# Kernel optimization log

Measured on AMD Instinct MI355X. Metric: run time of the kernel, lower is better.

Reference implementation:

```python
import jax, jax.numpy as jnp
import numpy as np
from jax import lax

BLANK = 1  # Offsets.GO
NEG = jnp.float32(-1e30)  # finite stand-in for -inf (avoids inf-inf NaNs)


def setup_inputs() -> dict:
    key = jax.random.key(0)
    k1, k2 = jax.random.split(key)
    T, N, C, L = 4000, 128, 128, 256
    log_prob = jax.random.normal(k1, (T, N, C), dtype=jnp.float32)
    input_lengths = jnp.full((N,), T, dtype=jnp.int32)
    # labels in [3, C): avoid PAD=0, GO(blank)=1, EOS=2
    targets = jax.random.randint(k2, (N, L), 3, C, dtype=jnp.int32)
    target_lengths = jnp.full((N,), L, dtype=jnp.int32)
    return {"log_prob": log_prob, "input_lengths": input_lengths,
            "targets": targets, "target_lengths": target_lengths}


def reference(log_prob, input_lengths, targets, target_lengths):
    T, N, C = log_prob.shape
    L = targets.shape[1]
    S = 2 * L + 1  # extended label sequence: blanks interleaved
    lp = jax.nn.log_softmax(log_prob, axis=-1)  # (T, N, C)

    ext = jnp.full((N, S), BLANK, dtype=targets.dtype).at[:, 1::2].set(targets)  # (N, S)
    # skip transition s-2 -> s allowed iff ext[s] != blank and ext[s] != ext[s-2]
    skip = jnp.concatenate(
        [jnp.zeros((N, 2), bool),
         (ext[:, 2:] != ext[:, :-2]) & (ext[:, 2:] != BLANK)], axis=1)  # (N, S)

    bidx = jnp.arange(N)
    emit0 = lp[0, bidx[:, None], ext]  # (N, S)
    alpha0 = jnp.full((N, S), NEG).at[:, 0].set(emit0[:, 0]).at[:, 1].set(emit0[:, 1])

    def step(alpha, xs):
        lp_t, t = xs  # lp_t: (N, C)
        emit = lp_t[bidx[:, None], ext]  # (N, S)
        a1 = jnp.concatenate([jnp.full((N, 1), NEG), alpha[:, :-1]], axis=1)
        a2 = jnp.where(skip,
                       jnp.concatenate([jnp.full((N, 2), NEG), alpha[:, :-2]], axis=1),
                       NEG)
        new = jnp.logaddexp(jnp.logaddexp(alpha, a1), a2) + emit
        alpha = jnp.where((t < input_lengths)[:, None], new, alpha)
        return alpha, None

    alpha, _ = lax.scan(step, alpha0, (lp[1:], jnp.arange(1, T)))

    end = 2 * target_lengths  # index of final blank state per example
    ll = jnp.logaddexp(alpha[bidx, end], alpha[bidx, end - 1])
    loss = -ll  # per-example negative log-likelihood
    # zero_infinity: infinite (i.e. ~NEG-magnitude) losses become 0
    loss = jnp.where(jnp.isfinite(loss) & (jnp.abs(loss) < 1e29), loss, 0.0)
    return jnp.sum(loss)  # reduction_type='sum'
```

## Files before the change

### kernel.cpp

```cpp
#include <hip/hip_runtime.h>
#include <math.h>

#define CTC_BLANK 1
#define RBW 132

struct Pv { double pb, p1, p3, p5, p7; };

#define GATH(P, boff)                              \
  {                                                \
    P.pb = (double)rb[(boff) + CTC_BLANK];         \
    P.p1 = (double)rb[(boff) + i1];                \
    P.p3 = (double)rb[(boff) + i3];                \
    P.p5 = (double)rb[(boff) + i5];                \
    P.p7 = (double)rb[(boff) + i7];                \
  }

#define CTC_STEP(J, PC, PN, HMI, HMO)                                  \
  {                                                                    \
    const int boff = RBW * ((J) & 1);                                  \
    float ex = __expf(pre[J].x), ey = __expf(pre[J].y);                \
    *(float2*)&rb[boff + 2 * lane] = make_float2(ex, ey);              \
    {                                                                  \
      int tl_ = t0 + (J) + 9;                                          \
      if (tl_ > Tlast) tl_ = Tlast;                                    \
      pre[J] = *(const float2*)(lpn + (size_t)tl_ * NC + 2 * lane);    \
    }                                                                  \
    GATH(PN, boff);                                                    \
    double t7o = a[7];                                                 \
    a8 = (a8 + t7o * m63) * PC.pb;                                     \
    a[7] = fma(sk7, a[5], a[7] + a[6]) * PC.p7;                        \
    HMO = __shfl_up(a[7], 1);                                          \
    a[6] = (a[6] + a[5]) * PC.pb;                                      \
    a[5] = fma(sk5, a[3], a[5] + a[4]) * PC.p5;                        \
    a[4] = (a[4] + a[3]) * PC.pb;                                      \
    a[3] = fma(sk3, a[1], a[3] + a[2]) * PC.p3;                        \
    a[2] = (a[2] + a[1]) * PC.pb;                                      \
    double hh = HMI * lz;                                              \
    a[1] = fma(sk1, hh, a[1] + a[0]) * PC.p1;                          \
    a[0] = (a[0] + hh) * PC.pb;                                        \
  }

__global__ __launch_bounds__(512) void ctc_main(
    const float* __restrict__ lp, const int* __restrict__ ilen,
    const int* __restrict__ tgt, const int* __restrict__ tlen,
    int T, int N, int C, int L,
    double* __restrict__ ws_lse,
    double* __restrict__ ws_ll) {
  const int n = blockIdx.x;
  const int tid = threadIdx.x;
  const int wid = tid >> 6;
  const int lane = tid & 63;
  const int NC = N * C;
  const int Tn = ilen[n];

  if (wid == 4) return;

  if (wid != 0) {
    const int h = (wid < 4) ? (wid - 1) : (wid - 2);
    const int per = (T + 5) / 6;
    const int tb = h * per;
    int te = tb + per;
    if (te > Tn) te = Tn;
    const float* basen = lp + (size_t)n * C;
    double acc = 0.0;
    for (int t0b = tb; t0b < te; t0b += 64) {
      int t = t0b + lane;
      if (t < te) {
        const float4* rp = (const float4*)(basen + (size_t)t * NC);
        float sx = 0.f, sy = 0.f, sz = 0.f, sw = 0.f;
        const int c4n = C >> 2;
#pragma unroll 8
        for (int c4 = 0; c4 < c4n; ++c4) {
          float4 v = rp[c4];
          sx += __expf(v.x); sy += __expf(v.y);
          sz += __expf(v.z); sw += __expf(v.w);
        }
        acc += log((double)((sx + sy) + (sz + sw)));
      }
    }
#pragma unroll
    for (int off = 32; off; off >>= 1) acc += __shfl_xor(acc, off);
    if (lane == 0) ws_lse[n * 6 + h] = acc;
    return;
  }

  __shared__ float rb[2 * RBW];
  __shared__ double adump[513];

  const int tlv = tlen[n];
  const int gend = 2 * tlv;
  const int* tg = tgt + (size_t)n * L;

  if (lane == 0) { rb[128] = 0.f; rb[RBW + 128] = 0.f; }

  int i1, i3, i5, i7;
  double sk1, sk3, sk5, sk7;
  {
    int idx[4]; double sk[4];
#pragma unroll
    for (int q = 0; q < 4; ++q) {
      int s = 2 * q + 1;
      int g = lane * 8 + s;
      int k = (g - 1) >> 1;
      int kc = (k < L) ? k : (L - 1);
      int eidx = tg[kc];
      double skv = 0.;
      if (g >= 3) {
        int kp = k - 1; if (kp > L - 1) kp = L - 1;
        int ep = tg[kp];
        skv = (eidx != ep && eidx != CTC_BLANK) ? 1. : 0.;
      }
      if (g > gend) eidx = 128;
      idx[q] = eidx; sk[q] = skv;
    }
    i1 = idx[0]; i3 = idx[1]; i5 = idx[2]; i7 = idx[3];
    sk1 = sk[0]; sk3 = sk[1]; sk5 = sk[2]; sk7 = sk[3];
  }
  const double m63 = (lane == 63) ? 1.0 : 0.0;
  const double lz  = (lane == 0) ? 0.0 : 1.0;

  const float* lpn = lp + (size_t)n * C;
  const int Tlast = T - 1;

  {
    float2 v0 = *(const float2*)(lpn + 2 * lane);
    *(float2*)&rb[2 * lane] = make_float2(__expf(v0.x), __expf(v0.y));
    int t1 = (1 > Tlast) ? Tlast : 1;
    float2 v1 = *(const float2*)(lpn + (size_t)t1 * NC + 2 * lane);
    *(float2*)&rb[RBW + 2 * lane] = make_float2(__expf(v1.x), __expf(v1.y));
  }

  Pv pA, pB;
  double a[8], a8 = 0.0;
  GATH(pA, 0);
  a[0] = (lane == 0) ? pA.pb : 0.0;
  a[1] = (lane == 0) ? pA.p1 : 0.0;
#pragma unroll
  for (int s = 2; s < 8; ++s) a[s] = 0.0;
  GATH(pA, RBW);

  float2 pre[8];
#pragma unroll
  for (int j = 0; j < 8; ++j) {
    int tl_ = 2 + j; if (tl_ > Tlast) tl_ = Tlast;
    pre[j] = *(const float2*)(lpn + (size_t)tl_ * NC + 2 * lane);
  }

  double hA = 0.0, hB = 0.0;
  long long Esum = 0;
  int t0 = 1;

  for (; t0 + 8 <= Tn; t0 += 8) {
    CTC_STEP(0, pA, pB, hA, hB)
    CTC_STEP(1, pB, pA, hB, hA)
    CTC_STEP(2, pA, pB, hA, hB)
    CTC_STEP(3, pB, pA, hB, hA)
    CTC_STEP(4, pA, pB, hA, hB)
    CTC_STEP(5, pB, pA, hB, hA)
    CTC_STEP(6, pA, pB, hA, hB)
    CTC_STEP(7, pB, pA, hB, hA)
    double m = fmax(a[0], a[1]);
    m = fmax(m, fmax(a[2], a[3]));
    m = fmax(m, fmax(a[4], a[5]));
    m = fmax(m, fmax(a[6], a[7]));
    m = fmax(m, a8);
    int hi = __double2hiint(m);
    int mx = __builtin_amdgcn_readlane(hi, 0);
#pragma unroll
    for (int l = 4; l < 64; l += 4) {
      int v = __builtin_amdgcn_readlane(hi, l);
      mx = (v > mx) ? v : mx;
    }
    int E = ((mx >> 20) & 0x7ff) - 1023;
    double sc = ldexp(1.0, -E);
    Esum += E;
#pragma unroll
    for (int s = 0; s < 8; ++s) a[s] *= sc;
    a8 *= sc;
    hA *= sc;
  }
  if (t0 + 0 < Tn) CTC_STEP(0, pA, pB, hA, hB)
  if (t0 + 1 < Tn) CTC_STEP(1, pB, pA, hB, hA)
  if (t0 + 2 < Tn) CTC_STEP(2, pA, pB, hA, hB)
  if (t0 + 3 < Tn) CTC_STEP(3, pB, pA, hB, hA)
  if (t0 + 4 < Tn) CTC_STEP(4, pA, pB, hA, hB)
  if (t0 + 5 < Tn) CTC_STEP(5, pB, pA, hB, hA)
  if (t0 + 6 < Tn) CTC_STEP(6, pA, pB, hA, hB)

#pragma unroll
  for (int s = 0; s < 8; ++s) adump[lane * 8 + s] = a[s];
  if (lane == 63) adump[512] = a8;
  if (lane == 0) {
    int end = gend;
    int i2 = (end > 0) ? (end - 1) : (2 * L);
    double Ae = adump[end] + adump[i2];
    ws_ll[n] = log(Ae) + (double)Esum * 0.69314718055994530942;
  }
}

__global__ void ctc_final(const double* __restrict__ ws_lse,
                          const double* __restrict__ ws_ll,
                          float* __restrict__ out, int N) {
  __shared__ double sred[128];
  const int i = threadIdx.x;
  double l = 0.0;
  if (i < N) {
    double denom = 0.0;
#pragma unroll
    for (int h = 0; h < 6; ++h) denom += ws_lse[i * 6 + h];
    double ll = ws_ll[i] - denom;
    double ls = -ll;
    if (!isfinite(ls) || fabs(ls) >= 1e29) ls = 0.0;
    l = ls;
  }
  sred[i] = l;
  __syncthreads();
#pragma unroll
  for (int off = 64; off > 0; off >>= 1) {
    if (i < off) sred[i] += sred[i + off];
    __syncthreads();
  }
  if (i == 0) out[0] = (float)sred[0];
}

extern "C" void kernel_launch(void* const* d_in, const int* in_sizes, int n_in,
                              void* d_out, int out_size, void* d_ws, size_t ws_size,
                              hipStream_t stream) {
  (void)n_in; (void)out_size; (void)ws_size;
  const float* lp = (const float*)d_in[0];
  const int* ilen = (const int*)d_in[1];
  const int* tgt = (const int*)d_in[2];
  const int* tlen = (const int*)d_in[3];

  const int N = in_sizes[1];
  const int L = in_sizes[2] / N;
  const int C = 128;
  const int T = in_sizes[0] / (N * C);

  double* ws_lse = (double*)d_ws;
  double* ws_ll = ws_lse + (size_t)N * 6;

  ctc_main<<<N, 512, 0, stream>>>(lp, ilen, tgt, tlen, T, N, C, L, ws_lse, ws_ll);
  ctc_final<<<1, 128, 0, stream>>>(ws_lse, ws_ll, (float*)d_out, N);
}
```

Baseline: 480.9 us.

## Deepen emission ring buffer, unroll 16 steps, DPP wave-max rescale

Grows the shared emission ring buffer from 2 to 4 slots so each step gathers emissions written two steps earlier, and moves the exp/store/prefetch after the recurrence, taking LDS latency off the serial alpha chain. The main loop is unrolled to 16 steps, which halves how often the rescale runs. The rescale now uses an integer max on exponent bits, a DPP wave reduction instead of 16 readlanes, and builds the scale factor directly rather than calling ldexp. This costs more register pressure and code size. Rescaling every 16 steps instead of 8 also leaves more room for double underflow.

```diff
diff --git a/kernel.cpp b/kernel.cpp
--- a/kernel.cpp
+++ b/kernel.cpp
@@ -5,6 +5,19 @@
 #define RBW 132
 
 struct Pv { double pb, p1, p3, p5, p7; };
+
+__device__ __forceinline__ int imax2(int a, int b) { return a > b ? a : b; }
+
+__device__ __forceinline__ int wave_imax_dpp(int v) {
+  int t;
+  t = __builtin_amdgcn_update_dpp(0, v, 0x111, 0xF, 0xF, true); v = imax2(v, t);
+  t = __builtin_amdgcn_update_dpp(0, v, 0x112, 0xF, 0xF, true); v = imax2(v, t);
+  t = __builtin_amdgcn_update_dpp(0, v, 0x114, 0xF, 0xF, true); v = imax2(v, t);
+  t = __builtin_amdgcn_update_dpp(0, v, 0x118, 0xF, 0xF, true); v = imax2(v, t);
+  t = __builtin_amdgcn_update_dpp(0, v, 0x142, 0xF, 0xF, true); v = imax2(v, t);
+  t = __builtin_amdgcn_update_dpp(0, v, 0x143, 0xF, 0xF, true); v = imax2(v, t);
+  return __builtin_amdgcn_readlane(v, 63);
+}
 
 #define GATH(P, boff)                              \
   {                                                \
@@ -15,29 +28,29 @@
     P.p7 = (double)rb[(boff) + i7];                \
   }
 
-#define CTC_STEP(J, PC, PN, HMI, HMO)                                  \
-  {                                                                    \
-    const int boff = RBW * ((J) & 1);                                  \
-    float ex = __expf(pre[J].x), ey = __expf(pre[J].y);                \
-    *(float2*)&rb[boff + 2 * lane] = make_float2(ex, ey);              \
-    {                                                                  \
-      int tl_ = t0 + (J) + 9;                                          \
-      if (tl_ > Tlast) tl_ = Tlast;                                    \
-      pre[J] = *(const float2*)(lpn + (size_t)tl_ * NC + 2 * lane);    \
-    }                                                                  \
-    GATH(PN, boff);                                                    \
-    double t7o = a[7];                                                 \
-    a8 = (a8 + t7o * m63) * PC.pb;                                     \
-    a[7] = fma(sk7, a[5], a[7] + a[6]) * PC.p7;                        \
-    HMO = __shfl_up(a[7], 1);                                          \
-    a[6] = (a[6] + a[5]) * PC.pb;                                      \
-    a[5] = fma(sk5, a[3], a[5] + a[4]) * PC.p5;                        \
-    a[4] = (a[4] + a[3]) * PC.pb;                                      \
-    a[3] = fma(sk3, a[1], a[3] + a[2]) * PC.p3;                        \
-    a[2] = (a[2] + a[1]) * PC.pb;                                      \
-    double hh = HMI * lz;                                              \
-    a[1] = fma(sk1, hh, a[1] + a[0]) * PC.p1;                          \
-    a[0] = (a[0] + hh) * PC.pb;                                        \
+#define CTC_STEP(J, PC, PN, HMI, HMO)                                    \
+  {                                                                      \
+    GATH(PN, RBW * (((J) + 2) & 3));                                     \
+    double t7s = (lane == 63) ? a[7] : 0.0;                              \
+    double hh = (lane == 0) ? 0.0 : HMI;                                 \
+    a8 = (a8 + t7s) * PC.pb;                                             \
+    a[7] = fma(sk7, a[5], a[7] + a[6]) * PC.p7;                          \
+    HMO = __shfl_up(a[7], 1);                                            \
+    a[6] = (a[6] + a[5]) * PC.pb;                                        \
+    a[5] = fma(sk5, a[3], a[5] + a[4]) * PC.p5;                          \
+    a[4] = (a[4] + a[3]) * PC.pb;                                        \
+    a[3] = fma(sk3, a[1], a[3] + a[2]) * PC.p3;                          \
+    a[2] = (a[2] + a[1]) * PC.pb;                                        \
+    a[1] = fma(sk1, hh, a[1] + a[0]) * PC.p1;                            \
+    a[0] = (a[0] + hh) * PC.pb;                                          \
+    {                                                                    \
+      float ex = __expf(pre[(J) & 7].x), ey = __expf(pre[(J) & 7].y);    \
+      *(float2*)&rb[RBW * (((J) + 3) & 3) + 2 * lane] =                  \
+          make_float2(ex, ey);                                           \
+      int tl_ = t0 + (J) + 10;                                           \
+      if (tl_ > Tlast) tl_ = Tlast;                                      \
+      pre[(J) & 7] = *(const float2*)(lpn + (size_t)tl_ * NC + 2 * lane);\
+    }                                                                    \
   }
 
 __global__ __launch_bounds__(512) void ctc_main(
@@ -84,14 +97,14 @@
     return;
   }
 
-  __shared__ float rb[2 * RBW];
+  __shared__ float rb[4 * RBW];
   __shared__ double adump[513];
 
   const int tlv = tlen[n];
   const int gend = 2 * tlv;
   const int* tg = tgt + (size_t)n * L;
 
-  if (lane == 0) { rb[128] = 0.f; rb[RBW + 128] = 0.f; }
+  if (lane < 4) rb[lane * RBW + 128] = 0.f;
 
   int i1, i3, i5, i7;
   double sk1, sk3, sk5, sk7;
@@ -116,18 +129,15 @@
     i1 = idx[0]; i3 = idx[1]; i5 = idx[2]; i7 = idx[3];
     sk1 = sk[0]; sk3 = sk[1]; sk5 = sk[2]; sk7 = sk[3];
   }
-  const double m63 = (lane == 63) ? 1.0 : 0.0;
-  const double lz  = (lane == 0) ? 0.0 : 1.0;
 
   const float* lpn = lp + (size_t)n * C;
   const int Tlast = T - 1;
 
-  {
-    float2 v0 = *(const float2*)(lpn + 2 * lane);
-    *(float2*)&rb[2 * lane] = make_float2(__expf(v0.x), __expf(v0.y));
-    int t1 = (1 > Tlast) ? Tlast : 1;
-    float2 v1 = *(const float2*)(lpn + (size_t)t1 * NC + 2 * lane);
-    *(float2*)&rb[RBW + 2 * lane] = make_float2(__expf(v1.x), __expf(v1.y));
+#pragma unroll
+  for (int r = 0; r < 3; ++r) {
+    int tr = (r > Tlast) ? Tlast : r;
+    float2 v = *(const float2*)(lpn + (size_t)tr * NC + 2 * lane);
+    *(float2*)&rb[r * RBW + 2 * lane] = make_float2(__expf(v.x), __expf(v.y));
   }
 
   Pv pA, pB;
@@ -142,7 +152,7 @@
   float2 pre[8];
 #pragma unroll
   for (int j = 0; j < 8; ++j) {
-    int tl_ = 2 + j; if (tl_ > Tlast) tl_ = Tlast;
+    int tl_ = 3 + j; if (tl_ > Tlast) tl_ = Tlast;
     pre[j] = *(const float2*)(lpn + (size_t)tl_ * NC + 2 * lane);
   }
 
@@ -150,42 +160,56 @@
   long long Esum = 0;
   int t0 = 1;
 
-  for (; t0 + 8 <= Tn; t0 += 8) {
-    CTC_STEP(0, pA, pB, hA, hB)
-    CTC_STEP(1, pB, pA, hB, hA)
-    CTC_STEP(2, pA, pB, hA, hB)
-    CTC_STEP(3, pB, pA, hB, hA)
-    CTC_STEP(4, pA, pB, hA, hB)
-    CTC_STEP(5, pB, pA, hB, hA)
-    CTC_STEP(6, pA, pB, hA, hB)
-    CTC_STEP(7, pB, pA, hB, hA)
-    double m = fmax(a[0], a[1]);
-    m = fmax(m, fmax(a[2], a[3]));
-    m = fmax(m, fmax(a[4], a[5]));
-    m = fmax(m, fmax(a[6], a[7]));
-    m = fmax(m, a8);
-    int hi = __double2hiint(m);
-    int mx = __builtin_amdgcn_readlane(hi, 0);
-#pragma unroll
-    for (int l = 4; l < 64; l += 4) {
-      int v = __builtin_amdgcn_readlane(hi, l);
-      mx = (v > mx) ? v : mx;
-    }
+  for (; t0 + 16 <= Tn; t0 += 16) {
+    CTC_STEP(0,  pA, pB, hA, hB)
+    CTC_STEP(1,  pB, pA, hB, hA)
+    CTC_STEP(2,  pA, pB, hA, hB)
+    CTC_STEP(3,  pB, pA, hB, hA)
+    CTC_STEP(4,  pA, pB, hA, hB)
+    CTC_STEP(5,  pB, pA, hB, hA)
+    CTC_STEP(6,  pA, pB, hA, hB)
+    CTC_STEP(7,  pB, pA, hB, hA)
+    CTC_STEP(8,  pA, pB, hA, hB)
+    CTC_STEP(9,  pB, pA, hB, hA)
+    CTC_STEP(10, pA, pB, hA, hB)
+    CTC_STEP(11, pB, pA, hB, hA)
+    CTC_STEP(12, pA, pB, hA, hB)
+    CTC_STEP(13, pB, pA, hB, hA)
+    CTC_STEP(14, pA, pB, hA, hB)
+    CTC_STEP(15, pB, pA, hB, hA)
+    int hi = __double2hiint(a[0]);
+    hi = imax2(hi, __double2hiint(a[1]));
+    hi = imax2(hi, __double2hiint(a[2]));
+    hi = imax2(hi, __double2hiint(a[3]));
+    hi = imax2(hi, __double2hiint(a[4]));
+    hi = imax2(hi, __double2hiint(a[5]));
+    hi = imax2(hi, __double2hiint(a[6]));
+    hi = imax2(hi, __double2hiint(a[7]));
+    hi = imax2(hi, __double2hiint(a8));
+    int mx = wave_imax_dpp(hi);
     int E = ((mx >> 20) & 0x7ff) - 1023;
-    double sc = ldexp(1.0, -E);
+    double sc = __hiloint2double((1023 - E) << 20, 0);
     Esum += E;
 #pragma unroll
     for (int s = 0; s < 8; ++s) a[s] *= sc;
     a8 *= sc;
     hA *= sc;
   }
-  if (t0 + 0 < Tn) CTC_STEP(0, pA, pB, hA, hB)
-  if (t0 + 1 < Tn) CTC_STEP(1, pB, pA, hB, hA)
-  if (t0 + 2 < Tn) CTC_STEP(2, pA, pB, hA, hB)
-  if (t0 + 3 < Tn) CTC_STEP(3, pB, pA, hB, hA)
-  if (t0 + 4 < Tn) CTC_STEP(4, pA, pB, hA, hB)
-  if (t0 + 5 < Tn) CTC_STEP(5, pB, pA, hB, hA)
-  if (t0 + 6 < Tn) CTC_STEP(6, pA, pB, hA, hB)
+  if (t0 + 0  < Tn) CTC_STEP(0,  pA, pB, hA, hB)
+  if (t0 + 1  < Tn) CTC_STEP(1,  pB, pA, hB, hA)
+  if (t0 + 2  < Tn) CTC_STEP(2,  pA, pB, hA, hB)
+  if (t0 + 3  < Tn) CTC_STEP(3,  pB, pA, hB, hA)
+  if (t0 + 4  < Tn) CTC_STEP(4,  pA, pB, hA, hB)
+  if (t0 + 5  < Tn) CTC_STEP(5,  pB, pA, hB, hA)
+  if (t0 + 6  < Tn) CTC_STEP(6,  pA, pB, hA, hB)
+  if (t0 + 7  < Tn) CTC_STEP(7,  pB, pA, hB, hA)
+  if (t0 + 8  < Tn) CTC_STEP(8,  pA, pB, hA, hB)
+  if (t0 + 9  < Tn) CTC_STEP(9,  pB, pA, hB, hA)
+  if (t0 + 10 < Tn) CTC_STEP(10, pA, pB, hA, hB)
+  if (t0 + 11 < Tn) CTC_STEP(11, pB, pA, hB, hA)
+  if (t0 + 12 < Tn) CTC_STEP(12, pA, pB, hA, hB)
+  if (t0 + 13 < Tn) CTC_STEP(13, pB, pA, hB, hA)
+  if (t0 + 14 < Tn) CTC_STEP(14, pA, pB, hA, hB)
 
 #pragma unroll
   for (int s = 0; s < 8; ++s) adump[lane * 8 + s] = a[s];
```

Measured after the change: 512.8 us. +6.6%, slower.
